# Kernel tuning notes

Hardware: AMD Instinct MI355X
Metric: run time of the kernel (lower is better)

## Reference

```python
import jax, jax.numpy as jnp
import numpy as np
import math

D_MODEL = 2048
N_HEADS = 16
D_HEAD = D_MODEL // N_HEADS

def setup_inputs() -> dict:
    key = jax.random.key(0)
    ks = jax.random.split(key, 6)
    B, S, D = 4, 2048, D_MODEL
    scale = 1.0 / math.sqrt(D)
    x  = jax.random.normal(ks[0], (B, S, D), dtype=jnp.float32)
    Wq = jax.random.normal(ks[1], (D, D), dtype=jnp.float32) * scale
    Wk = jax.random.normal(ks[2], (D, D), dtype=jnp.float32) * scale
    Wv = jax.random.normal(ks[3], (D, D), dtype=jnp.float32) * scale
    Wo = jax.random.normal(ks[4], (D, D), dtype=jnp.float32) * scale
    bo = jax.random.normal(ks[5], (D,), dtype=jnp.float32) * 0.01
    return {"x": x, "Wq": Wq, "Wk": Wk, "Wv": Wv, "Wo": Wo, "bo": bo}

def reference(x, Wq, Wk, Wv, Wo, bo):
    B, S, D = x.shape
    H, Dh = N_HEADS, D_HEAD
    # projections (bias=False for q/k/v); torch Linear: y = x @ W^T
    q = (x @ Wq.T).reshape(B, S, H, Dh).transpose(0, 2, 1, 3)  # [B,H,S,Dh]
    k = (x @ Wk.T).reshape(B, S, H, Dh).transpose(0, 2, 1, 3)
    v = (x @ Wv.T).reshape(B, S, H, Dh).transpose(0, 2, 1, 3)
    scores = jnp.einsum('bhqd,bhkd->bhqk', q, k) / math.sqrt(Dh)  # [B,H,S,S]
    causal = jnp.tril(jnp.ones((S, S), dtype=bool))
    scores = jnp.where(causal, scores, -jnp.inf)
    attn = jax.nn.softmax(scores, axis=-1)
    # dropout p=0.0 -> identity (eval)
    out = jnp.einsum('bhqk,bhkd->bhqd', attn, v)  # [B,H,S,Dh]
    out = out.transpose(0, 2, 1, 3).reshape(B, S, D)
    return out @ Wo.T + bo
```

## Files before the change

kernel.cpp:

```cpp
#include <hip/hip_runtime.h>
#include <stdint.h>

#define D_MODEL 2048
#define NH 16
#define DH 128
#define BATCH 4
#define SEQ 2048
#define MTOT (BATCH*SEQ)
#define LDQ 6144

typedef __bf16 bf16x8 __attribute__((ext_vector_type(8)));
typedef float f32x4 __attribute__((ext_vector_type(4)));
typedef short short8 __attribute__((ext_vector_type(8)));

static __device__ __forceinline__ unsigned short f2bf(float f) {
  union { float f; unsigned int u; } v; v.f = f;
  return (unsigned short)((v.u + 0x7FFFu + ((v.u >> 16) & 1u)) >> 16);
}

#define FENCEM() asm volatile("" ::: "memory")
#define GBAR() do { FENCEM(); __builtin_amdgcn_s_barrier(); FENCEM(); } while (0)

__global__ __launch_bounds__(256) void cvt_all_k(const float* __restrict__ x,
                                                 const float* __restrict__ w0, const float* __restrict__ w1,
                                                 const float* __restrict__ w2, const float* __restrict__ w3,
                                                 unsigned short* __restrict__ xo,
                                                 unsigned short* __restrict__ wo_cat,
                                                 unsigned short* __restrict__ wo_o) {
  const size_t WSZ = (size_t)D_MODEL * D_MODEL;
  int id = blockIdx.x;
  const float* src; unsigned short* dst; int lo;
  if (id < 8192) { src = x; dst = xo; lo = id; }
  else {
    int wsel = (id - 8192) >> 11;
    lo = (id - 8192) & 2047;
    switch (wsel) {
      case 0: src = w0; dst = wo_cat; break;
      case 1: src = w1; dst = wo_cat + WSZ; break;
      case 2: src = w2; dst = wo_cat + 2 * WSZ; break;
      default: src = w3; dst = wo_o; break;
    }
  }
  int i = (lo * 256 + threadIdx.x) * 8;
  float4 a = *(const float4*)(src + i);
  float4 b = *(const float4*)(src + i + 4);
  union { unsigned short u[8]; short8 v; } o;
  o.u[0] = f2bf(a.x); o.u[1] = f2bf(a.y); o.u[2] = f2bf(a.z); o.u[3] = f2bf(a.w);
  o.u[4] = f2bf(b.x); o.u[5] = f2bf(b.y); o.u[6] = f2bf(b.z); o.u[7] = f2bf(b.w);
  *(short8*)(dst + i) = o.v;
}

template<bool OUT_BF16, bool ADD_BIAS>
__global__ __launch_bounds__(512, 2) void gemm256(const unsigned short* __restrict__ A,
                                                  const unsigned short* __restrict__ B,
                                                  void* __restrict__ C,
                                                  const float* __restrict__ bias,
                                                  int M, int N, int K) {
  __shared__ __align__(16) unsigned short As[256 * 64];
  __shared__ __align__(16) unsigned short Bs[256 * 64];

  const int tid = threadIdx.x;
  const int lane = tid & 63;
  const int l15 = lane & 15, l4 = lane >> 4;
  const int wid = tid >> 6;
  const int wr = wid >> 2, wc = wid & 3;

  const int gx = gridDim.x;
  const int id = blockIdx.y * gx + blockIdx.x;
  const int msl = gx >> 2;
  const int nsl = gridDim.y >> 1;
  const int xcd = id & 7;
  const int lid = id >> 3;
  const int bm = (xcd >> 1) * msl + lid / nsl;
  const int bn = (xcd & 1) * nsl + lid % nsl;

  const int NT = K >> 6;

  const int st_r = tid >> 3;
  const int st_c = (tid & 7) ^ (st_r & 7);
  const int st_ld = st_r * 64 + (tid & 7) * 8;

#define STAGE_A(t, h) do { \
  _Pragma("unroll") \
  for (int _i = 0; _i < 2; ++_i) { \
    const unsigned short* _g = A + (size_t)(bm * 256 + (h) * 128 + _i * 64 + st_r) * K + (t) * 64 + st_c * 8; \
    __builtin_amdgcn_global_load_lds((const __attribute__((address_space(1))) void*)_g, \
        (__attribute__((address_space(3))) void*)(&As[(h) * 8192 + _i * 4096 + st_ld]), 16, 0, 0); \
  } \
} while (0)

#define STAGE_B(t, h) do { \
  _Pragma("unroll") \
  for (int _i = 0; _i < 2; ++_i) { \
    const unsigned short* _g = B + (size_t)(bn * 256 + (h) * 128 + _i * 64 + st_r) * K + (t) * 64 + st_c * 8; \
    __builtin_amdgcn_global_load_lds((const __attribute__((address_space(1))) void*)_g, \
        (__attribute__((address_space(3))) void*)(&Bs[(h) * 8192 + _i * 4096 + st_ld]), 16, 0, 0); \
  } \
} while (0)

#define LDA_F(dst, mh) do { \
  _Pragma("unroll") \
  for (int _mi = 0; _mi < 4; ++_mi) { \
    int _row = wr * 128 + (mh) * 64 + _mi * 16 + l15; \
    _Pragma("unroll") \
    for (int _kk = 0; _kk < 2; ++_kk) \
      dst[_mi][_kk] = *(const bf16x8*)&As[_row * 64 + ((_kk * 4 + l4) ^ (l15 & 7)) * 8]; \
  } \
} while (0)

#define LDB_F(dst, nq) do { \
  _Pragma("unroll") \
  for (int _ni = 0; _ni < 2; ++_ni) { \
    int _row = wc * 64 + (nq) * 32 + _ni * 16 + l15; \
    _Pragma("unroll") \
    for (int _kk = 0; _kk < 2; ++_kk) \
      dst[_ni][_kk] = *(const bf16x8*)&Bs[_row * 64 + ((_kk * 4 + l4) ^ (l15 & 7)) * 8]; \
  } \
} while (0)

#define PHASE_MFMA(MH, NQ, BFR) do { \
  _Pragma("unroll") \
  for (int _mi = 0; _mi < 4; ++_mi) { \
    _Pragma("unroll") \
    for (int _ni = 0; _ni < 2; ++_ni) { \
      acc[(MH) * 4 + _mi][(NQ) * 2 + _ni] = __builtin_amdgcn_mfma_f32_16x16x32_bf16( \
          af[_mi][0], BFR[_ni][0], acc[(MH) * 4 + _mi][(NQ) * 2 + _ni], 0, 0, 0); \
      acc[(MH) * 4 + _mi][(NQ) * 2 + _ni] = __builtin_amdgcn_mfma_f32_16x16x32_bf16( \
          af[_mi][1], BFR[_ni][1], acc[(MH) * 4 + _mi][(NQ) * 2 + _ni], 0, 0, 0); \
    } \
  } \
} while (0)

  f32x4 acc[8][4] = {};

  STAGE_A(0, 0); STAGE_A(0, 1);
  STAGE_B(0, 0); STAGE_B(0, 1);
  asm volatile("s_waitcnt vmcnt(0)" ::: "memory");
  GBAR();

  for (int t = 0; t < NT; ++t) {
    bf16x8 af[4][2], bf0[2][2], bf1[2][2];

    LDA_F(af, 0);
    LDB_F(bf0, 0);
    LDB_F(bf1, 1);
    __builtin_amdgcn_s_setprio(1);
    PHASE_MFMA(0, 0, bf0);
    PHASE_MFMA(0, 1, bf1);
    __builtin_amdgcn_s_setprio(0);

    LDA_F(af, 1);
    asm volatile("s_waitcnt lgkmcnt(0)" ::: "memory");
    GBAR();

    if (t + 1 < NT) { STAGE_A(t + 1, 0); STAGE_A(t + 1, 1);
                      STAGE_B(t + 1, 0); STAGE_B(t + 1, 1); }
    __builtin_amdgcn_s_setprio(1);
    PHASE_MFMA(1, 1, bf1);
    PHASE_MFMA(1, 0, bf0);
    __builtin_amdgcn_s_setprio(0);
    asm volatile("s_waitcnt vmcnt(0)" ::: "memory");
    GBAR();
  }

  const int row0 = bm * 256 + wr * 128;
  const int col0 = bn * 256 + wc * 64;
#pragma unroll
  for (int mi = 0; mi < 8; ++mi) {
#pragma unroll
    for (int ni = 0; ni < 4; ++ni) {
      int col = col0 + ni * 16 + l15;
#pragma unroll
      for (int r = 0; r < 4; ++r) {
        int row = row0 + mi * 16 + l4 * 4 + r;
        float v = acc[mi][ni][r];
        if (ADD_BIAS) v += bias[col];
        if (OUT_BF16)
          ((unsigned short*)C)[(size_t)row * N + col] = f2bf(v);
        else
          ((float*)C)[(size_t)row * N + col] = v;
      }
    }
  }
#undef STAGE_A
#undef STAGE_B
#undef LDA_F
#undef LDB_F
#undef PHASE_MFMA
}

__global__ __launch_bounds__(256, 2) void attn_k(const unsigned short* __restrict__ Qp,
                                                 const unsigned short* __restrict__ Kp,
                                                 const unsigned short* __restrict__ Vp,
                                                 unsigned short* __restrict__ O) {
  __shared__ __align__(16) unsigned short Ks[2][64 * 128];
  __shared__ __align__(16) unsigned short Vt[2][128 * 64];
  __shared__ __align__(16) unsigned int   Pl[4][32 * 32];

  const int tid = threadIdx.x;
  const int lane = tid & 63;
  const int l15 = lane & 15, l4 = lane >> 4;
  const int w = tid >> 6;

  const int idx = blockIdx.y * gridDim.x + blockIdx.x;
  const int x8 = idx & 7, j = idx >> 3;
  const int bh = x8 * 8 + (j & 7);
  const int qt = 15 - (j >> 3);
  const int b = bh >> 4, h = bh & 15;

  const size_t baseI = (size_t)b * SEQ * LDQ + (size_t)h * DH;
  const size_t baseO = (size_t)b * SEQ * D_MODEL + (size_t)h * DH;
  const int qw = qt * 128 + w * 32;

  bf16x8 qf[2][4];
#pragma unroll
  for (int qg = 0; qg < 2; ++qg) {
    const unsigned short* qptr = Qp + baseI + (size_t)(qw + qg * 16 + l15) * LDQ;
#pragma unroll
    for (int kk = 0; kk < 4; ++kk)
      qf[qg][kk] = *(const bf16x8*)(qptr + kk * 32 + l4 * 8);
  }

  f32x4 acc[2][8] = {};
  float m_run[2] = {-3.4028235e38f, -3.4028235e38f};
  float lp[2] = {0.f, 0.f};
  const float SC = 0.12751743f;

  short8 vreg[4];
  const int nkt = 2 * qt + 2;

  const int vkp0 = tid >> 4, vch0 = tid & 15;
  const int vkp1 = (tid + 256) >> 4, vch1 = vch0;

#pragma unroll
  for (int it = 0; it < 4; ++it) {
    int c = tid + it * 256;
    int key = c >> 4, pos = c & 15;
    int gchunk = pos ^ (key & 7);
    const unsigned short* ga = Kp + baseI + (size_t)key * LDQ + gchunk * 8;
    __builtin_amdgcn_global_load_lds((const __attribute__((address_space(1))) void*)ga,
                                     (__attribute__((address_space(3))) void*)(&Ks[0][c * 8]),
                                     16, 0, 0);
  }
  FENCEM();
  {
    const unsigned short* gv0 = Vp + baseI + (size_t)(2 * vkp0) * LDQ + vch0 * 8;
    vreg[0] = *(const short8*)(gv0);
    vreg[1] = *(const short8*)(gv0 + LDQ);
    const unsigned short* gv1 = Vp + baseI + (size_t)(2 * vkp1) * LDQ + vch1 * 8;
    vreg[2] = *(const short8*)(gv1);
    vreg[3] = *(const short8*)(gv1 + LDQ);
  }

  for (int kt = 0; kt < nkt; ++kt) {
    const int cur = kt & 1;
    const int kv0 = kt * 64;
    const bool act = (kv0 <= qw + 31);

    asm volatile("s_waitcnt vmcnt(4)" ::: "memory");
    GBAR();

    f32x4 sacc[2][4] = {};
    if (act) {
      __builtin_amdgcn_s_setprio(1);
#pragma unroll
      for (int st = 0; st < 4; ++st) {
        int key = st * 16 + l15;
#pragma unroll
        for (int kk = 0; kk < 4; ++kk) {
          bf16x8 kf = *(const bf16x8*)&Ks[cur][key * 128 + ((kk * 32 + l4 * 8) ^ ((key & 7) << 3))];
          sacc[0][st] = __builtin_amdgcn_mfma_f32_16x16x32_bf16(kf, qf[0][kk], sacc[0][st], 0, 0, 0);
          sacc[1][st] = __builtin_amdgcn_mfma_f32_16x16x32_bf16(kf, qf[1][kk], sacc[1][st], 0, 0, 0);
        }
      }
      __builtin_amdgcn_s_setprio(0);
    }
    FENCEM();

    if (kt + 1 < nkt) {
      const int kn0 = kv0 + 64;
      const int nb = cur ^ 1;
#pragma unroll
      for (int it = 0; it < 4; ++it) {
        int c = tid + it * 256;
        int key = c >> 4, pos = c & 15;
        int gchunk = pos ^ (key & 7);
        const unsigned short* ga = Kp + baseI + (size_t)(kn0 + key) * LDQ + gchunk * 8;
        __builtin_amdgcn_global_load_lds((const __attribute__((address_space(1))) void*)ga,
                                         (__attribute__((address_space(3))) void*)(&Ks[nb][c * 8]),
                                         16, 0, 0);
      }
      asm volatile("s_waitcnt vmcnt(4)" ::: "memory");
    } else {
      asm volatile("s_waitcnt vmcnt(0)" ::: "memory");
    }

#pragma unroll
    for (int i = 0; i < 2; ++i) {
      int kp = i ? vkp1 : vkp0;
      int ch = i ? vch1 : vch0;
      union { short8 v; unsigned short u[8]; } ua, ub;
      ua.v = vreg[2 * i]; ub.v = vreg[2 * i + 1];
#pragma unroll
      for (int j2 = 0; j2 < 8; ++j2) {
        int dh = ch * 8 + j2;
        int sv = (ch ^ j2) & 7;
        unsigned val = (unsigned)ua.u[j2] | ((unsigned)ub.u[j2] << 16);
        *(unsigned int*)&Vt[cur][dh * 64 + ((2 * kp) ^ (sv << 3))] = val;
      }
    }
    if (kt + 1 < nkt) {
      const int kn0 = kv0 + 64;
      const unsigned short* gv0 = Vp + baseI + (size_t)(kn0 + 2 * vkp0) * LDQ + vch0 * 8;
      vreg[0] = *(const short8*)(gv0);
      vreg[1] = *(const short8*)(gv0 + LDQ);
      const unsigned short* gv1 = Vp + baseI + (size_t)(kn0 + 2 * vkp1) * LDQ + vch1 * 8;
      vreg[2] = *(const short8*)(gv1);
      vreg[3] = *(const short8*)(gv1 + LDQ);
    }
    __syncthreads();

    if (act) {
      const bool tail = (kv0 + 63 > qw);
      float tmax[2];
#pragma unroll
      for (int qg = 0; qg < 2; ++qg) {
        if (tail) {
          int q = qw + qg * 16 + l15;
#pragma unroll
          for (int st = 0; st < 4; ++st)
#pragma unroll
            for (int r = 0; r < 4; ++r) {
              int key = kv0 + st * 16 + l4 * 4 + r;
              if (key > q) sacc[qg][st][r] = -3.0e38f;
            }
        }
        float a0 = fmaxf(fmaxf(sacc[qg][0][0], sacc[qg][0][1]), fmaxf(sacc[qg][0][2], sacc[qg][0][3]));
        float a1 = fmaxf(fmaxf(sacc[qg][1][0], sacc[qg][1][1]), fmaxf(sacc[qg][1][2], sacc[qg][1][3]));
        float a2 = fmaxf(fmaxf(sacc[qg][2][0], sacc[qg][2][1]), fmaxf(sacc[qg][2][2], sacc[qg][2][3]));
        float a3 = fmaxf(fmaxf(sacc[qg][3][0], sacc[qg][3][1]), fmaxf(sacc[qg][3][2], sacc[qg][3][3]));
        float t = fmaxf(fmaxf(a0, a1), fmaxf(a2, a3));
        t = fmaxf(t, __shfl_xor(t, 16));
        t = fmaxf(t, __shfl_xor(t, 32));
        tmax[qg] = t;
      }
      bool grow = (tmax[0] > m_run[0] + 8.f) || (tmax[1] > m_run[1] + 8.f);
      if (__any(grow)) {
#pragma unroll
        for (int qg = 0; qg < 2; ++qg) {
          float nm = fmaxf(m_run[qg], tmax[qg]);
          float scl = __builtin_amdgcn_exp2f((m_run[qg] - nm) * SC);
          m_run[qg] = nm;
          lp[qg] *= scl;
#pragma unroll
          for (int r = 0; r < 4; ++r) {
            float srow = __shfl(scl, l4 * 4 + r);
#pragma unroll
            for (int df = 0; df < 8; ++df) acc[qg][df][r] *= srow;
          }
        }
      }
#pragma unroll
      for (int qg = 0; qg < 2; ++qg) {
        int q = qg * 16 + l15;
        float ps = 0.f;
#pragma unroll
        for (int st = 0; st < 4; ++st) {
          float p0 = __builtin_amdgcn_exp2f((sacc[qg][st][0] - m_run[qg]) * SC);
          float p1 = __builtin_amdgcn_exp2f((sacc[qg][st][1] - m_run[qg]) * SC);
          float p2 = __builtin_amdgcn_exp2f((sacc[qg][st][2] - m_run[qg]) * SC);
          float p3 = __builtin_amdgcn_exp2f((sacc[qg][st][3] - m_run[qg]) * SC);
          ps += (p0 + p1) + (p2 + p3);
          unsigned w0 = (unsigned)f2bf(p0) | ((unsigned)f2bf(p1) << 16);
          unsigned w1 = (unsigned)f2bf(p2) | ((unsigned)f2bf(p3) << 16);
          int kw0 = st * 8 + l4 * 2;
          Pl[w][q * 32 + (kw0 ^ ((q & 7) << 2))] = w0;
          Pl[w][q * 32 + ((kw0 + 1) ^ ((q & 7) << 2))] = w1;
        }
        lp[qg] += ps;
      }
      __builtin_amdgcn_s_setprio(1);
#pragma unroll
      for (int ks2 = 0; ks2 < 2; ++ks2) {
        int kwb = ks2 * 16 + l4 * 4;
        bf16x8 pa0 = *(const bf16x8*)&Pl[w][l15 * 32 + (kwb ^ ((l15 & 7) << 2))];
        bf16x8 pa1 = *(const bf16x8*)&Pl[w][(16 + l15) * 32 + (kwb ^ ((l15 & 7) << 2))];
#pragma unroll
        for (int df = 0; df < 8; ++df) {
          int dh = df * 16 + l15;
          int sv = ((dh >> 3) ^ dh) & 7;
          bf16x8 vb = *(const bf16x8*)&Vt[cur][dh * 64 + ((ks2 * 32 + l4 * 8) ^ (sv << 3))];
          acc[0][df] = __builtin_amdgcn_mfma_f32_16x16x32_bf16(pa0, vb, acc[0][df], 0, 0, 0);
          acc[1][df] = __builtin_amdgcn_mfma_f32_16x16x32_bf16(pa1, vb, acc[1][df], 0, 0, 0);
        }
      }
      __builtin_amdgcn_s_setprio(0);
    }
  }

#pragma unroll
  for (int qg = 0; qg < 2; ++qg) {
    float t = lp[qg];
    t += __shfl_xor(t, 16);
    t += __shfl_xor(t, 32);
    float linv = 1.0f / t;
#pragma unroll
    for (int r = 0; r < 4; ++r) {
      float lrow = __shfl(linv, l4 * 4 + r);
      int row = qw + qg * 16 + l4 * 4 + r;
#pragma unroll
      for (int df = 0; df < 8; ++df)
        O[baseO + (size_t)row * D_MODEL + df * 16 + l15] = f2bf(acc[qg][df][r] * lrow);
    }
  }
}

extern "C" void kernel_launch(void* const* d_in, const int* in_sizes, int n_in,
                              void* d_out, int out_size, void* d_ws, size_t ws_size,
                              hipStream_t stream) {
  const float* x  = (const float*)d_in[0];
  const float* Wq = (const float*)d_in[1];
  const float* Wk = (const float*)d_in[2];
  const float* Wv = (const float*)d_in[3];
  const float* Wo = (const float*)d_in[4];
  const float* bo = (const float*)d_in[5];
  float* out = (float*)d_out;

  unsigned short* ws = (unsigned short*)d_ws;
  const size_t XSZ = (size_t)MTOT * D_MODEL;
  const size_t WSZ = (size_t)D_MODEL * D_MODEL;
  unsigned short* xb   = ws;
  unsigned short* Wcat = xb + XSZ;
  unsigned short* Wob  = Wcat + 3 * WSZ;
  unsigned short* QKV  = Wob + WSZ;
  unsigned short* AOb  = xb;

  cvt_all_k<<<16384, 256, 0, stream>>>(x, Wq, Wk, Wv, Wo, xb, Wcat, Wob);

  dim3 gq(MTOT / 256, LDQ / 256);
  gemm256<true, false><<<gq, 512, 0, stream>>>(xb, Wcat, QKV, nullptr, MTOT, LDQ, D_MODEL);

  dim3 ga(SEQ / 128, BATCH * NH);
  attn_k<<<ga, 256, 0, stream>>>(QKV, QKV + 2048, QKV + 4096, AOb);

  dim3 gg(MTOT / 256, D_MODEL / 256);
  gemm256<false, true><<<gg, 512, 0, stream>>>(AOb, Wob, out, bo, MTOT, D_MODEL, D_MODEL);
}
```

Baseline: 397.1 us.

## Double-buffer GEMM LDS tiles and prefetch A two K-steps ahead

The 256x256 GEMM tile now keeps two LDS buffers for A and B. The A tile for step t+2 and the B tile for step t+1 are issued during step t, and vmcnt is relaxed so global-to-LDS copies overlap MFMA work instead of draining at every iteration. This doubles the shared memory per block to 128 KB. With only about 160 KB of LDS per CU, that likely cuts residency from the requested 2 blocks per CU to 1, which can offset the overlap gain.

```diff
diff --git a/kernel.cpp b/kernel.cpp
--- a/kernel.cpp
+++ b/kernel.cpp
@@ -56,8 +56,8 @@
                                                   void* __restrict__ C,
                                                   const float* __restrict__ bias,
                                                   int M, int N, int K) {
-  __shared__ __align__(16) unsigned short As[256 * 64];
-  __shared__ __align__(16) unsigned short Bs[256 * 64];
+  __shared__ __align__(16) unsigned short As[2][256 * 64];
+  __shared__ __align__(16) unsigned short Bs[2][256 * 64];
 
   const int tid = threadIdx.x;
   const int lane = tid & 63;
@@ -81,40 +81,42 @@
   const int st_ld = st_r * 64 + (tid & 7) * 8;
 
 #define STAGE_A(t, h) do { \
+  const int _b = (t) & 1; \
   _Pragma("unroll") \
   for (int _i = 0; _i < 2; ++_i) { \
     const unsigned short* _g = A + (size_t)(bm * 256 + (h) * 128 + _i * 64 + st_r) * K + (t) * 64 + st_c * 8; \
     __builtin_amdgcn_global_load_lds((const __attribute__((address_space(1))) void*)_g, \
-        (__attribute__((address_space(3))) void*)(&As[(h) * 8192 + _i * 4096 + st_ld]), 16, 0, 0); \
+        (__attribute__((address_space(3))) void*)(&As[_b][(h) * 8192 + _i * 4096 + st_ld]), 16, 0, 0); \
   } \
 } while (0)
 
 #define STAGE_B(t, h) do { \
+  const int _b = (t) & 1; \
   _Pragma("unroll") \
   for (int _i = 0; _i < 2; ++_i) { \
     const unsigned short* _g = B + (size_t)(bn * 256 + (h) * 128 + _i * 64 + st_r) * K + (t) * 64 + st_c * 8; \
     __builtin_amdgcn_global_load_lds((const __attribute__((address_space(1))) void*)_g, \
-        (__attribute__((address_space(3))) void*)(&Bs[(h) * 8192 + _i * 4096 + st_ld]), 16, 0, 0); \
+        (__attribute__((address_space(3))) void*)(&Bs[_b][(h) * 8192 + _i * 4096 + st_ld]), 16, 0, 0); \
   } \
 } while (0)
 
-#define LDA_F(dst, mh) do { \
+#define LDA_F(dst, bufb, mh) do { \
   _Pragma("unroll") \
   for (int _mi = 0; _mi < 4; ++_mi) { \
     int _row = wr * 128 + (mh) * 64 + _mi * 16 + l15; \
     _Pragma("unroll") \
     for (int _kk = 0; _kk < 2; ++_kk) \
-      dst[_mi][_kk] = *(const bf16x8*)&As[_row * 64 + ((_kk * 4 + l4) ^ (l15 & 7)) * 8]; \
+      dst[_mi][_kk] = *(const bf16x8*)&As[bufb][_row * 64 + ((_kk * 4 + l4) ^ (l15 & 7)) * 8]; \
   } \
 } while (0)
 
-#define LDB_F(dst, nq) do { \
+#define LDB_F(dst, bufb, nq) do { \
   _Pragma("unroll") \
   for (int _ni = 0; _ni < 2; ++_ni) { \
     int _row = wc * 64 + (nq) * 32 + _ni * 16 + l15; \
     _Pragma("unroll") \
     for (int _kk = 0; _kk < 2; ++_kk) \
-      dst[_ni][_kk] = *(const bf16x8*)&Bs[_row * 64 + ((_kk * 4 + l4) ^ (l15 & 7)) * 8]; \
+      dst[_ni][_kk] = *(const bf16x8*)&Bs[bufb][_row * 64 + ((_kk * 4 + l4) ^ (l15 & 7)) * 8]; \
   } \
 } while (0)
 
@@ -135,31 +137,35 @@
 
   STAGE_A(0, 0); STAGE_A(0, 1);
   STAGE_B(0, 0); STAGE_B(0, 1);
-  asm volatile("s_waitcnt vmcnt(0)" ::: "memory");
+  if (NT > 1) { STAGE_A(1, 0); STAGE_A(1, 1); }
+  if (NT > 1) asm volatile("s_waitcnt vmcnt(4)" ::: "memory");
+  else        asm volatile("s_waitcnt vmcnt(0)" ::: "memory");
   GBAR();
 
   for (int t = 0; t < NT; ++t) {
+    const int bufb = t & 1;
     bf16x8 af[4][2], bf0[2][2], bf1[2][2];
 
-    LDA_F(af, 0);
-    LDB_F(bf0, 0);
-    LDB_F(bf1, 1);
+    LDA_F(af, bufb, 0);
+    LDB_F(bf0, bufb, 0);
+    LDB_F(bf1, bufb, 1);
+    if (t + 1 < NT) { STAGE_B(t + 1, 0); STAGE_B(t + 1, 1); }
     __builtin_amdgcn_s_setprio(1);
     PHASE_MFMA(0, 0, bf0);
     PHASE_MFMA(0, 1, bf1);
     __builtin_amdgcn_s_setprio(0);
 
-    LDA_F(af, 1);
+    LDA_F(af, bufb, 1);
     asm volatile("s_waitcnt lgkmcnt(0)" ::: "memory");
     GBAR();
 
-    if (t + 1 < NT) { STAGE_A(t + 1, 0); STAGE_A(t + 1, 1);
-                      STAGE_B(t + 1, 0); STAGE_B(t + 1, 1); }
+    if (t + 2 < NT) { STAGE_A(t + 2, 0); STAGE_A(t + 2, 1); }
     __builtin_amdgcn_s_setprio(1);
     PHASE_MFMA(1, 1, bf1);
     PHASE_MFMA(1, 0, bf0);
     __builtin_amdgcn_s_setprio(0);
-    asm volatile("s_waitcnt vmcnt(0)" ::: "memory");
+    if (t + 2 < NT) asm volatile("s_waitcnt vmcnt(4)" ::: "memory");
+    else            asm volatile("s_waitcnt vmcnt(0)" ::: "memory");
     GBAR();
   }
 
```

Result: faster. 388.6 us, median of 2 (-2.1%).
